# Kernel optimization log

Hardware: AMD Instinct MI355X
Metric: run time of the kernel (lower is better)

The kernel has to match this reference:

```python
import jax, jax.numpy as jnp
import numpy as np

ID, IH, IW = 8, 16, 16
HEADS, DIM_HEAD = 8, 32
N = ID * IH * IW  # 2048
INNER = HEADS * DIM_HEAD  # 256
TABLE = (2 * ID - 1) * (2 * IH - 1) * (2 * IW - 1)  # 14415


def _relative_index():
    # Faithful replication of the torch buffer computation (including its
    # unconventional offsets: dim2 never offset, dim1 never scaled).
    g = np.meshgrid(np.arange(ID), np.arange(IH), np.arange(IW), indexing='ij')
    coords = np.stack(g).reshape(3, -1)  # (3, N)
    rc = coords[:, :, None] - coords[:, None, :]  # (3, N, N)
    rc = rc.copy()
    rc[0] += (IH - 1) + (ID - 1)
    rc[1] += (IW - 1) + (ID - 1)
    rc[0] *= 2 * IH - 1
    rel = rc.transpose(1, 2, 0).sum(-1).reshape(-1)  # (N*N,)
    return jnp.asarray(rel, dtype=jnp.int32)


def setup_inputs() -> dict:
    key = jax.random.key(0)
    k1, k2, k3, k4, k5 = jax.random.split(key, 5)
    B, C = 4, 256
    x = jax.random.normal(k1, (B, N, C), dtype=jnp.float32)
    w_qkv = jax.random.normal(k2, (C, 3 * INNER), dtype=jnp.float32) * (C ** -0.5)
    bias_table = jax.random.normal(k3, (TABLE, HEADS), dtype=jnp.float32) * 0.02
    w_out = jax.random.normal(k4, (INNER, C), dtype=jnp.float32) * (INNER ** -0.5)
    b_out = jax.random.normal(k5, (C,), dtype=jnp.float32) * 0.02
    return {"x": x, "w_qkv": w_qkv, "bias_table": bias_table,
            "w_out": w_out, "b_out": b_out, "rel_index": _relative_index()}


def reference(x, w_qkv, bias_table, w_out, b_out, rel_index):
    B, n, C = x.shape
    scale = DIM_HEAD ** -0.5
    qkv = x @ w_qkv  # (B, N, 3*h*d)
    qkv = qkv.reshape(B, n, 3, HEADS, DIM_HEAD)
    q = qkv[:, :, 0].transpose(0, 2, 1, 3)  # (B, h, N, d)
    k = qkv[:, :, 1].transpose(0, 2, 1, 3)
    v = qkv[:, :, 2].transpose(0, 2, 1, 3)
    attn = jnp.einsum('bhnd,bhmd->bhnm', q * scale, k)  # (B, h, N, N)
    bias = bias_table[rel_index].reshape(n, n, HEADS).transpose(2, 0, 1)  # (h, N, N)
    attn = jax.nn.softmax(attn + bias[None], axis=-1)
    out = jnp.einsum('bhnm,bhmd->bhnd', attn, v)  # (B, h, N, d)
    out = out.transpose(0, 2, 1, 3).reshape(B, n, INNER)
    return out @ w_out + b_out
```

## Files before the change

kernel.cpp:

```cpp
#include <hip/hip_runtime.h>
#include <hip/hip_bf16.h>
#include <hip/hip_fp16.h>

#define NTOK 2048
#define HEADS 8
#define DHEAD 32
#define CDIM 256
#define BATCH 4

typedef _Float16 f16x8 __attribute__((ext_vector_type(8)));
typedef _Float16 f16x4 __attribute__((ext_vector_type(4)));
typedef float f32x4 __attribute__((ext_vector_type(4)));
typedef __fp16 fp16v2 __attribute__((ext_vector_type(2)));

static __device__ inline f16x4 pack4(float a, float b, float c, float d) {
    fp16v2 lo = __builtin_amdgcn_cvt_pkrtz(a, b);
    fp16v2 hi = __builtin_amdgcn_cvt_pkrtz(c, d);
    union { struct { fp16v2 lo, hi; } p; f16x4 v; } u;
    u.p.lo = lo; u.p.hi = hi;
    return u.v;
}

static __device__ inline f16x8 pack8f(float a, float b, float c, float d,
                                      float e, float f, float g2, float h2) {
    union { struct { fp16v2 a, b, c, d; } p; f16x8 v; } u;
    u.p.a = __builtin_amdgcn_cvt_pkrtz(a, b);
    u.p.b = __builtin_amdgcn_cvt_pkrtz(c, d);
    u.p.c = __builtin_amdgcn_cvt_pkrtz(e, f);
    u.p.d = __builtin_amdgcn_cvt_pkrtz(g2, h2);
    return u.v;
}

static __device__ inline f16x8 pack8(float4 a, float4 b) {
    return pack8f(a.x, a.y, a.z, a.w, b.x, b.y, b.z, b.w);
}

__global__ __launch_bounds__(256) void prep(const float* __restrict__ x,
                                            const float* __restrict__ w_qkv,
                                            const float* __restrict__ w_out,
                                            _Float16* __restrict__ xh,
                                            _Float16* __restrict__ wqkvT,
                                            _Float16* __restrict__ woutT) {
    __shared__ float tl[32][33];
    const int bid = blockIdx.x;
    if (bid < 1024) {
        const int id = bid * 256 + threadIdx.x;
        const int row = id >> 5;
        const int c = id & 31;
        const int kt = c >> 2;
        const int g = c & 3;
        const float4 a = *(const float4*)(x + row * 256 + kt * 32 + g * 8);
        const float4 b = *(const float4*)(x + row * 256 + kt * 32 + g * 8 + 4);
        const int dst = (row >> 4) * 4096 + kt * 512 + (g * 16 + (row & 15)) * 8;
        *(f16x8*)(xh + dst) = pack8(a, b);
    } else if (bid < 1216) {
        const int t = bid - 1024;
        const int kt = t / 24, nt = t - kt * 24;
        const int tx = threadIdx.x & 31, ty = threadIdx.x >> 5;
#pragma unroll
        for (int i = 0; i < 4; ++i) {
            const int r = ty + i * 8;
            tl[r][tx] = w_qkv[(kt * 32 + r) * 768 + nt * 32 + tx];
        }
        __syncthreads();
        if (threadIdx.x < 128) {
            const int nl = threadIdx.x & 31;
            const int g2 = threadIdx.x >> 5;
            const int ntile = (nt * 32 + nl) >> 4;
            const int lane = (nl & 15) + 16 * g2;
            const float* col = &tl[g2 * 8][nl];
            *(f16x8*)(wqkvT + (ntile * 8 + kt) * 512 + lane * 8) =
                pack8f(col[0], col[33], col[66], col[99],
                       col[132], col[165], col[198], col[231]);
        }
    } else {
        const int t = bid - 1216;
        const int kt = t >> 3, nt = t & 7;
        const int tx = threadIdx.x & 31, ty = threadIdx.x >> 5;
#pragma unroll
        for (int i = 0; i < 4; ++i) {
            const int r = ty + i * 8;
            tl[r][tx] = w_out[(kt * 32 + r) * 256 + nt * 32 + tx];
        }
        __syncthreads();
        if (threadIdx.x < 128) {
            const int nl = threadIdx.x & 31;
            const int g2 = threadIdx.x >> 5;
            const int ntile = (nt * 32 + nl) >> 4;
            const int lane = (nl & 15) + 16 * g2;
            const float* col = &tl[g2 * 8][nl];
            *(f16x8*)(woutT + (ntile * 8 + kt) * 512 + lane * 8) =
                pack8f(col[0], col[33], col[66], col[99],
                       col[132], col[165], col[198], col[231]);
        }
    }
}

__global__ __launch_bounds__(256) void qkv_gemm(const _Float16* __restrict__ xh,
                                                const _Float16* __restrict__ wT,
                                                _Float16* __restrict__ qb,
                                                _Float16* __restrict__ kb,
                                                _Float16* __restrict__ vT) {
    __shared__ _Float16 vt_s[64 * 72];
    const int wave = threadIdx.x >> 6;
    const int lane = threadIdx.x & 63;
    const int idx16 = lane & 15;
    const int g = lane >> 4;

    const int m_base = blockIdx.x * 64;
    const int n0 = blockIdx.y * 64 + wave * 16;

    f32x4 acc[4] = {{0.f, 0.f, 0.f, 0.f}, {0.f, 0.f, 0.f, 0.f},
                    {0.f, 0.f, 0.f, 0.f}, {0.f, 0.f, 0.f, 0.f}};

    const _Float16* bp = wT + (size_t)(blockIdx.y * 4 + wave) * 4096 + lane * 8;
    const _Float16* ap = xh + (size_t)(blockIdx.x * 4) * 4096 + lane * 8;

    for (int kt = 0; kt < 8; ++kt) {
        const f16x8 bf = *(const f16x8*)(bp + kt * 512);
#pragma unroll
        for (int m = 0; m < 4; ++m) {
            const f16x8 af = *(const f16x8*)(ap + m * 4096 + kt * 512);
            acc[m] = __builtin_amdgcn_mfma_f32_16x16x32_f16(af, bf, acc[m], 0, 0, 0);
        }
    }

    const int b = m_base >> 11;
    const int nb = m_base & 2047;
    if (blockIdx.y < 8) {
        const int c = n0 + idx16;
        const int which = c >> 8;
        const int h = (c >> 5) & 7;
        const int d = c & 31;
#pragma unroll
        for (int m = 0; m < 4; ++m) {
#pragma unroll
            for (int r = 0; r < 4; ++r) {
                const int n = nb + m * 16 + g * 4 + r;
                const float val = acc[m][r];
                if (which == 0) {
                    qb[((b * HEADS + h) * NTOK + n) * DHEAD + d] =
                        (_Float16)(val * 0.2550565444545147f);
                } else {
                    kb[((b * HEADS + h) * NTOK + n) * DHEAD + d] = (_Float16)val;
                }
            }
        }
    } else {
        const int cp = wave * 16 + idx16;
#pragma unroll
        for (int m = 0; m < 4; ++m) {
            const int kl = m * 16 + g * 4;
            const int dst = (kl & 32) + (((kl >> 2) & 3) << 3) +
                            (((kl >> 4) & 1) << 2);
            *(f16x4*)(vt_s + cp * 72 + dst) =
                pack4(acc[m][0], acc[m][1], acc[m][2], acc[m][3]);
        }
        __syncthreads();
        const int cpo = threadIdx.x >> 2;
        const int part = threadIdx.x & 3;
        const int vidx = (blockIdx.y - 8) * 64 + cpo;
        const int hh = vidx >> 5;
        const int d = vidx & 31;
        const _Float16* src = vt_s + cpo * 72 + part * 16;
        _Float16* dst = vT + ((size_t)(b * HEADS + hh) * DHEAD + d) * NTOK +
                        nb + part * 16;
        *(f16x8*)(dst) = *(const f16x8*)(src);
        *(f16x8*)(dst + 8) = *(const f16x8*)(src + 8);
    }
}

__global__ __launch_bounds__(256, 2) void attn_full(
    const _Float16* __restrict__ qp, const _Float16* __restrict__ kp,
    const _Float16* __restrict__ vT, const float* __restrict__ bias_table,
    _Float16* __restrict__ aout) {
    __shared__ float ft[4096];
    __shared__ f16x8 sbuf_v[1024];
    char* sbuf = (char*)sbuf_v;

    const int bh = blockIdx.x;
    const int h = bh & 7;
    for (int u = threadIdx.x; u < 1024; u += 256) {
        const float v =
            bias_table[(1023 - u) * HEADS + h] * 1.4426950408889634f - 8.0f;
        ft[4 * u] = v;
        if (u >= 1) ft[4 * u - 3] = v;
        if (u >= 2) ft[4 * u - 6] = v;
        if (u >= 3) ft[4 * u - 9] = v;
    }

    const int wave = threadIdx.x >> 6;
    const int lane = threadIdx.x & 63;
    const int qi = lane & 15;
    const int g = lane >> 4;
    const int q0 = blockIdx.y * 256 + wave * 64;

    const int tid = threadIdx.x;
    const bool isK = tid < 128;
    const int st_row = (tid & 127) >> 2;
    const int st_c16 = tid & 3;
    const int st_dst = (isK ? 0 : 2048) + st_row * 64 +
                       ((st_c16 ^ ((st_row >> 1) & 3)) << 4);
    const _Float16* st_src = isK
        ? kp + ((size_t)bh * NTOK + st_row) * DHEAD + st_c16 * 8
        : vT + ((size_t)bh * DHEAD + st_row) * NTOK + st_c16 * 8;
    const int st_stride = isK ? 32 * DHEAD : 32;

    const int swz = (qi >> 1) & 3;
    const int kf0_off = qi * 64 + ((g ^ swz) << 4);
    const int kf1_off = kf0_off + 1024;
    const int va_lo_off = 2048 + qi * 64 + ((g ^ swz) << 4);
    const int va_hi_off = va_lo_off + 1024;

    const int ig0 = q0 + qi;
    const int ib0 = 31 * (ig0 >> 8) + ((ig0 >> 4) & 15) + (ig0 & 15) + 704;
    const int ub0 = 1023 - ib0 + 4 * g;

    f16x8 qf[4];
#pragma unroll
    for (int m = 0; m < 4; ++m)
        qf[m] = *(const f16x8*)(qp + (bh * NTOK + q0 + m * 16 + qi) * DHEAD + g * 8);

    f32x4 acc0[4] = {{0.f, 0.f, 0.f, 0.f}, {0.f, 0.f, 0.f, 0.f},
                     {0.f, 0.f, 0.f, 0.f}, {0.f, 0.f, 0.f, 0.f}};
    f32x4 acc1[4] = {{0.f, 0.f, 0.f, 0.f}, {0.f, 0.f, 0.f, 0.f},
                     {0.f, 0.f, 0.f, 0.f}, {0.f, 0.f, 0.f, 0.f}};
    f32x4 accl[4] = {{0.f, 0.f, 0.f, 0.f}, {0.f, 0.f, 0.f, 0.f},
                     {0.f, 0.f, 0.f, 0.f}, {0.f, 0.f, 0.f, 0.f}};
    const f16x8 ones8 = {(_Float16)1.f, (_Float16)1.f, (_Float16)1.f,
                         (_Float16)1.f, (_Float16)1.f, (_Float16)1.f,
                         (_Float16)1.f, (_Float16)1.f};

    f16x8 stg0 = *(const f16x8*)(st_src);
    f16x8 stg1 = *(const f16x8*)(st_src + st_stride);
    *(f16x8*)(sbuf + st_dst) = stg0;
    *(f16x8*)(sbuf + 4096 + st_dst) = stg1;
    __syncthreads();

    int cur = 0;
    for (int kt2 = 0; kt2 < 32; ++kt2) {
        if (kt2 < 31) {
            stg0 = *(const f16x8*)(st_src + (2 * kt2 + 2) * st_stride);
            stg1 = *(const f16x8*)(st_src + (2 * kt2 + 3) * st_stride);
        }

#pragma unroll
        for (int tp = 0; tp < 2; ++tp) {
            const int kbase = (kt2 * 2 + tp) * 32;
            const char* bs = sbuf + cur * 8192 + tp * 4096;
            const f16x8 kf0 = *(const f16x8*)(bs + kf0_off);
            const f16x8 kf1 = *(const f16x8*)(bs + kf1_off);
            const f16x8 va_lo = *(const f16x8*)(bs + va_lo_off);
            const f16x8 va_hi = *(const f16x8*)(bs + va_hi_off);

            const int koff = 31 * (kbase >> 8) + ((kbase >> 4) & 15);
            const int u0 = ub0 + koff;

            __builtin_amdgcn_s_setprio(1);
#pragma unroll
            for (int m = 0; m < 4; ++m) {
                const f32x4 c0 = *(const f32x4*)&ft[(u0 - m) << 2];
                const f32x4 c1 = *(const f32x4*)&ft[(u0 - m + 1) << 2];
                f32x4 s0 = __builtin_amdgcn_mfma_f32_16x16x32_f16(kf0, qf[m], c0, 0, 0, 0);
                f32x4 s1 = __builtin_amdgcn_mfma_f32_16x16x32_f16(kf1, qf[m], c1, 0, 0, 0);

                const float p0 = __builtin_amdgcn_exp2f(s0[0]);
                const float p1 = __builtin_amdgcn_exp2f(s0[1]);
                const float p2 = __builtin_amdgcn_exp2f(s0[2]);
                const float p3 = __builtin_amdgcn_exp2f(s0[3]);
                const float p4 = __builtin_amdgcn_exp2f(s1[0]);
                const float p5 = __builtin_amdgcn_exp2f(s1[1]);
                const float p6 = __builtin_amdgcn_exp2f(s1[2]);
                const float p7 = __builtin_amdgcn_exp2f(s1[3]);

                const f16x8 pf = pack8f(p0, p1, p2, p3, p4, p5, p6, p7);

                acc0[m] = __builtin_amdgcn_mfma_f32_16x16x32_f16(va_lo, pf, acc0[m], 0, 0, 0);
                acc1[m] = __builtin_amdgcn_mfma_f32_16x16x32_f16(va_hi, pf, acc1[m], 0, 0, 0);
                accl[m] = __builtin_amdgcn_mfma_f32_16x16x32_f16(ones8, pf, accl[m], 0, 0, 0);
            }
            __builtin_amdgcn_s_setprio(0);
        }

        if (kt2 < 31) {
            *(f16x8*)(sbuf + (cur ^ 1) * 8192 + st_dst) = stg0;
            *(f16x8*)(sbuf + (cur ^ 1) * 8192 + 4096 + st_dst) = stg1;
        }
        __syncthreads();
        cur ^= 1;
    }

    char* ts = sbuf + wave * 4096;
#pragma unroll
    for (int m = 0; m < 4; ++m) {
        const float inv = 1.f / accl[m][0];
        const int row = m * 16 + qi;
        const int sw = row & 7;
        *(f16x4*)(ts + row * 64 + ((g ^ sw) << 3)) =
            pack4(acc0[m][0] * inv, acc0[m][1] * inv,
                  acc0[m][2] * inv, acc0[m][3] * inv);
        *(f16x4*)(ts + row * 64 + (((g + 4) ^ sw) << 3)) =
            pack4(acc1[m][0] * inv, acc1[m][1] * inv,
                  acc1[m][2] * inv, acc1[m][3] * inv);
    }
    __syncthreads();
    const int b = bh >> 3;
    const size_t abase = ((size_t)((b * NTOK + q0) >> 4) * 8 + h) * 512;
#pragma unroll
    for (int m = 0; m < 4; ++m) {
        const int row = m * 16 + qi;
        const int sw = row & 7;
        const f16x4 lo = *(const f16x4*)(ts + row * 64 + (((2 * g) ^ sw) << 3));
        const f16x4 hi = *(const f16x4*)(ts + row * 64 + (((2 * g + 1) ^ sw) << 3));
        union { struct { f16x4 lo, hi; } p; f16x8 v; } u;
        u.p.lo = lo; u.p.hi = hi;
        *(f16x8*)(aout + abase + m * 4096 + lane * 8) = u.v;
    }
}

__global__ __launch_bounds__(256) void out_gemm(const _Float16* __restrict__ aoutF,
                                                const _Float16* __restrict__ woutT,
                                                const float* __restrict__ b_out,
                                                float* __restrict__ out) {
    const int wave = threadIdx.x >> 6;
    const int lane = threadIdx.x & 63;
    const int idx16 = lane & 15;
    const int g = lane >> 4;
    const int m_base = blockIdx.x * 64;
    const int n0 = blockIdx.y * 64 + wave * 16;

    f32x4 acc[4] = {{0.f, 0.f, 0.f, 0.f}, {0.f, 0.f, 0.f, 0.f},
                    {0.f, 0.f, 0.f, 0.f}, {0.f, 0.f, 0.f, 0.f}};

    const _Float16* bp = woutT + (size_t)(blockIdx.y * 4 + wave) * 4096 + lane * 8;
    const _Float16* ap = aoutF + (size_t)(blockIdx.x * 4) * 4096 + lane * 8;

    for (int kt = 0; kt < 8; ++kt) {
        const f16x8 bf = *(const f16x8*)(bp + kt * 512);
#pragma unroll
        for (int m = 0; m < 4; ++m) {
            const f16x8 af = *(const f16x8*)(ap + m * 4096 + kt * 512);
            acc[m] = __builtin_amdgcn_mfma_f32_16x16x32_f16(af, bf, acc[m], 0, 0, 0);
        }
    }

    const int c = n0 + idx16;
    const float bias = b_out[c];
#pragma unroll
    for (int m = 0; m < 4; ++m) {
#pragma unroll
        for (int r = 0; r < 4; ++r) {
            const int tok = m_base + m * 16 + g * 4 + r;
            out[tok * 256 + c] = acc[m][r] + bias;
        }
    }
}

extern "C" void kernel_launch(void* const* d_in, const int* in_sizes, int n_in,
                              void* d_out, int out_size, void* d_ws, size_t ws_size,
                              hipStream_t stream) {
    const float* x = (const float*)d_in[0];
    const float* w_qkv = (const float*)d_in[1];
    const float* bias_table = (const float*)d_in[2];
    const float* w_out = (const float*)d_in[3];
    const float* b_out = (const float*)d_in[4];
    float* out = (float*)d_out;

    _Float16* aout = (_Float16*)d_ws;
    _Float16* qb = aout + 2097152;
    _Float16* kb = qb + 2097152;
    _Float16* vT = kb + 2097152;
    _Float16* wqkvT = vT + 2097152;
    _Float16* woutT = wqkvT + 196608;
    _Float16* xh = aout;

    prep<<<1280, 256, 0, stream>>>(x, w_qkv, w_out, xh, wqkvT, woutT);
    qkv_gemm<<<dim3(128, 12), 256, 0, stream>>>(xh, wqkvT, qb, kb, vT);
    attn_full<<<dim3(32, 8), 256, 0, stream>>>(qb, kb, vT, bias_table, aout);
    out_gemm<<<dim3(128, 4), 256, 0, stream>>>(aout, woutT, b_out, out);
}
```

Before: 65.13 us.

## Split attention over key halves and merge partials in output GEMM

The attention kernel is split along the key dimension into two halves via a third grid axis, doubling the number of blocks. Each block writes unnormalised fp16 partial outputs and fp32 row sums. The output GEMM adds the two partials and scales by the inverse of the combined sum before its MFMA. This works without a max-subtraction rescale because the kernel already uses a fixed offset instead of a running max. The aim is better occupancy on a launch of only 256 blocks, at the cost of extra partial-output traffic, fp16 accumulation of unnormalised sums, and more work in the output GEMM.

```diff
diff --git a/kernel.cpp b/kernel.cpp
--- a/kernel.cpp
+++ b/kernel.cpp
@@ -170,10 +170,10 @@
     }
 }
 
-__global__ __launch_bounds__(256, 2) void attn_full(
+__global__ __launch_bounds__(256, 4) void attn_partial(
     const _Float16* __restrict__ qp, const _Float16* __restrict__ kp,
     const _Float16* __restrict__ vT, const float* __restrict__ bias_table,
-    _Float16* __restrict__ aout) {
+    _Float16* __restrict__ paccF, float* __restrict__ pl) {
     __shared__ float ft[4096];
     __shared__ f16x8 sbuf_v[1024];
     char* sbuf = (char*)sbuf_v;
@@ -194,6 +194,8 @@
     const int qi = lane & 15;
     const int g = lane >> 4;
     const int q0 = blockIdx.y * 256 + wave * 64;
+    const int ks = blockIdx.z;
+    const int kstart = ks * 1024;
 
     const int tid = threadIdx.x;
     const bool isK = tid < 128;
@@ -202,8 +204,8 @@
     const int st_dst = (isK ? 0 : 2048) + st_row * 64 +
                        ((st_c16 ^ ((st_row >> 1) & 3)) << 4);
     const _Float16* st_src = isK
-        ? kp + ((size_t)bh * NTOK + st_row) * DHEAD + st_c16 * 8
-        : vT + ((size_t)bh * DHEAD + st_row) * NTOK + st_c16 * 8;
+        ? kp + ((size_t)bh * NTOK + kstart + st_row) * DHEAD + st_c16 * 8
+        : vT + ((size_t)bh * DHEAD + st_row) * NTOK + kstart + st_c16 * 8;
     const int st_stride = isK ? 32 * DHEAD : 32;
 
     const int swz = (qi >> 1) & 3;
@@ -238,15 +240,15 @@
     __syncthreads();
 
     int cur = 0;
-    for (int kt2 = 0; kt2 < 32; ++kt2) {
-        if (kt2 < 31) {
+    for (int kt2 = 0; kt2 < 16; ++kt2) {
+        if (kt2 < 15) {
             stg0 = *(const f16x8*)(st_src + (2 * kt2 + 2) * st_stride);
             stg1 = *(const f16x8*)(st_src + (2 * kt2 + 3) * st_stride);
         }
 
 #pragma unroll
         for (int tp = 0; tp < 2; ++tp) {
-            const int kbase = (kt2 * 2 + tp) * 32;
+            const int kbase = kstart + (kt2 * 2 + tp) * 32;
             const char* bs = sbuf + cur * 8192 + tp * 4096;
             const f16x8 kf0 = *(const f16x8*)(bs + kf0_off);
             const f16x8 kf1 = *(const f16x8*)(bs + kf1_off);
@@ -282,7 +284,7 @@
             __builtin_amdgcn_s_setprio(0);
         }
 
-        if (kt2 < 31) {
+        if (kt2 < 15) {
             *(f16x8*)(sbuf + (cur ^ 1) * 8192 + st_dst) = stg0;
             *(f16x8*)(sbuf + (cur ^ 1) * 8192 + 4096 + st_dst) = stg1;
         }
@@ -290,22 +292,22 @@
         cur ^= 1;
     }
 
+    const int part = bh * 2 + ks;
     char* ts = sbuf + wave * 4096;
 #pragma unroll
     for (int m = 0; m < 4; ++m) {
-        const float inv = 1.f / accl[m][0];
         const int row = m * 16 + qi;
         const int sw = row & 7;
         *(f16x4*)(ts + row * 64 + ((g ^ sw) << 3)) =
-            pack4(acc0[m][0] * inv, acc0[m][1] * inv,
-                  acc0[m][2] * inv, acc0[m][3] * inv);
+            pack4(acc0[m][0], acc0[m][1], acc0[m][2], acc0[m][3]);
         *(f16x4*)(ts + row * 64 + (((g + 4) ^ sw) << 3)) =
-            pack4(acc1[m][0] * inv, acc1[m][1] * inv,
-                  acc1[m][2] * inv, acc1[m][3] * inv);
+            pack4(acc1[m][0], acc1[m][1], acc1[m][2], acc1[m][3]);
+        if (g == 0) pl[part * NTOK + q0 + row] = accl[m][0];
     }
     __syncthreads();
     const int b = bh >> 3;
-    const size_t abase = ((size_t)((b * NTOK + q0) >> 4) * 8 + h) * 512;
+    const size_t abase = ((size_t)((b * NTOK + q0) >> 4) * 8 + h) * 512 +
+                         (size_t)ks * 2097152;
 #pragma unroll
     for (int m = 0; m < 4; ++m) {
         const int row = m * 16 + qi;
@@ -314,11 +316,12 @@
         const f16x4 hi = *(const f16x4*)(ts + row * 64 + (((2 * g + 1) ^ sw) << 3));
         union { struct { f16x4 lo, hi; } p; f16x8 v; } u;
         u.p.lo = lo; u.p.hi = hi;
-        *(f16x8*)(aout + abase + m * 4096 + lane * 8) = u.v;
-    }
-}
-
-__global__ __launch_bounds__(256) void out_gemm(const _Float16* __restrict__ aoutF,
+        *(f16x8*)(paccF + abase + m * 4096 + lane * 8) = u.v;
+    }
+}
+
+__global__ __launch_bounds__(256) void out_gemm(const _Float16* __restrict__ paccF,
+                                                const float* __restrict__ pl,
                                                 const _Float16* __restrict__ woutT,
                                                 const float* __restrict__ b_out,
                                                 float* __restrict__ out) {
@@ -328,18 +331,27 @@
     const int g = lane >> 4;
     const int m_base = blockIdx.x * 64;
     const int n0 = blockIdx.y * 64 + wave * 16;
+    const int b = m_base >> 11;
+    const int nb = m_base & 2047;
 
     f32x4 acc[4] = {{0.f, 0.f, 0.f, 0.f}, {0.f, 0.f, 0.f, 0.f},
                     {0.f, 0.f, 0.f, 0.f}, {0.f, 0.f, 0.f, 0.f}};
 
     const _Float16* bp = woutT + (size_t)(blockIdx.y * 4 + wave) * 4096 + lane * 8;
-    const _Float16* ap = aoutF + (size_t)(blockIdx.x * 4) * 4096 + lane * 8;
+    const _Float16* ap0 = paccF + (size_t)(blockIdx.x * 4) * 4096 + lane * 8;
+    const _Float16* ap1 = ap0 + 2097152;
 
     for (int kt = 0; kt < 8; ++kt) {
         const f16x8 bf = *(const f16x8*)(bp + kt * 512);
+        const int plbase = ((b * 8 + kt) * 2) * 2048 + nb;
 #pragma unroll
         for (int m = 0; m < 4; ++m) {
-            const f16x8 af = *(const f16x8*)(ap + m * 4096 + kt * 512);
+            const int n = m * 16 + idx16;
+            const float lv = pl[plbase + n] + pl[plbase + 2048 + n];
+            const _Float16 hinv = (_Float16)(1.0f / lv);
+            const f16x8 a0 = *(const f16x8*)(ap0 + m * 4096 + kt * 512);
+            const f16x8 a1 = *(const f16x8*)(ap1 + m * 4096 + kt * 512);
+            const f16x8 af = (a0 + a1) * hinv;
             acc[m] = __builtin_amdgcn_mfma_f32_16x16x32_f16(af, bf, acc[m], 0, 0, 0);
         }
     }
@@ -366,16 +378,18 @@
     const float* b_out = (const float*)d_in[4];
     float* out = (float*)d_out;
 
-    _Float16* aout = (_Float16*)d_ws;
-    _Float16* qb = aout + 2097152;
+    _Float16* paccF = (_Float16*)d_ws;
+    float* pl = (float*)(paccF + 4194304);
+    _Float16* qb = (_Float16*)(pl + 131072);
     _Float16* kb = qb + 2097152;
     _Float16* vT = kb + 2097152;
     _Float16* wqkvT = vT + 2097152;
     _Float16* woutT = wqkvT + 196608;
-    _Float16* xh = aout;
+    _Float16* xh = (_Float16*)paccF;
 
     prep<<<1280, 256, 0, stream>>>(x, w_qkv, w_out, xh, wqkvT, woutT);
     qkv_gemm<<<dim3(128, 12), 256, 0, stream>>>(xh, wqkvT, qb, kb, vT);
-    attn_full<<<dim3(32, 8), 256, 0, stream>>>(qb, kb, vT, bias_table, aout);
-    out_gemm<<<dim3(128, 4), 256, 0, stream>>>(aout, woutT, b_out, out);
-}
+    attn_partial<<<dim3(32, 8, 2), 256, 0, stream>>>(qb, kb, vT, bias_table,
+                                                     paccF, pl);
+    out_gemm<<<dim3(128, 4), 256, 0, stream>>>(paccF, pl, woutT, b_out, out);
+}
```

Result: faster. 60.38 us (-7.3%).
